# Kernel tuning notes

Measured on AMD Instinct MI355X. Metric: run time of the kernel, lower is better.

Reference implementation:

```python
import jax, jax.numpy as jnp
import numpy as np


def _lstm_scan(x, mask, W_ih, W_hh, h0, c0):
    # x: [B,S,D], mask: [B,S] bool. Masked LSTM (bias=False, PyTorch gate order i,f,g,o).
    def step(carry, inp):
        h, c = carry
        xt, mt = inp
        gates = xt @ W_ih.T + h @ W_hh.T          # [B, 4H]
        i, f, g, o = jnp.split(gates, 4, axis=-1)
        c_new = jax.nn.sigmoid(f) * c + jax.nn.sigmoid(i) * jnp.tanh(g)
        h_new = jax.nn.sigmoid(o) * jnp.tanh(c_new)
        m = mt[:, None]
        h = jnp.where(m, h_new, h)
        c = jnp.where(m, c_new, c)
        return (h, c), h
    (hT, cT), hs = jax.lax.scan(step, (h0, c0), (x.swapaxes(0, 1), mask.T))
    return hs.swapaxes(0, 1), hT, cT  # [B,S,H], [B,H], [B,H]


def setup_inputs() -> dict:
    key = jax.random.key(0)
    ks = jax.random.split(key, 24)
    B, S, V, E, H, DA, R, MH = 64, 1024, 50000, 300, 256, 64, 16, 512
    N_ET, N_PRT, N_POPT = 50, 12, 8
    sc = 1.0 / np.sqrt(H)
    input_ids = jax.random.randint(ks[0], (B, S), 0, V)
    len_li = jnp.sort(jax.random.randint(ks[1], (B,), S // 2, S + 1))[::-1]  # descending, >=1
    inp = {
        'input_ids': input_ids,
        'len_li': len_li,
        'h0': jnp.zeros((2, B, H), jnp.float32),
        'c0': jnp.zeros((2, B, H), jnp.float32),
        'emb': jax.random.normal(ks[2], (V, E), jnp.float32) * 0.1,
        'W_ih_f': jax.random.normal(ks[3], (4 * H, E), jnp.float32) * sc,
        'W_hh_f': jax.random.normal(ks[4], (4 * H, H), jnp.float32) * sc,
        'W_ih_b': jax.random.normal(ks[5], (4 * H, E), jnp.float32) * sc,
        'W_hh_b': jax.random.normal(ks[6], (4 * H, H), jnp.float32) * sc,
        'S1': jax.random.uniform(ks[7], (DA, 2 * H), jnp.float32, -0.1, 0.1),
        'S2': jax.random.uniform(ks[8], (R, DA), jnp.float32, -0.1, 0.1),
        'W_et': jax.random.uniform(ks[9], (MH, R * 2 * H), jnp.float32, -0.1, 0.1),
        'b_et': jnp.zeros((MH,), jnp.float32),
        'Wd_et': jax.random.uniform(ks[10], (N_ET, MH), jnp.float32, -0.1, 0.1),
        'bd_et': jnp.zeros((N_ET,), jnp.float32),
        'W_prt': jax.random.uniform(ks[11], (MH, R * 2 * H), jnp.float32, -0.1, 0.1),
        'b_prt': jnp.zeros((MH,), jnp.float32),
        'Wd_prt': jax.random.uniform(ks[12], (N_PRT, MH), jnp.float32, -0.1, 0.1),
        'bd_prt': jnp.zeros((N_PRT,), jnp.float32),
        'W_popt': jax.random.uniform(ks[13], (MH, R * 2 * H), jnp.float32, -0.1, 0.1),
        'b_popt': jnp.zeros((MH,), jnp.float32),
        'Wd_popt': jax.random.uniform(ks[14], (N_POPT, MH), jnp.float32, -0.1, 0.1),
        'bd_popt': jnp.zeros((N_POPT,), jnp.float32),
    }
    return inp


def reference(input_ids, len_li, h0, c0, emb, W_ih_f, W_hh_f, W_ih_b, W_hh_b,
              S1, S2, W_et, b_et, Wd_et, bd_et, W_prt, b_prt, Wd_prt, bd_prt,
              W_popt, b_popt, Wd_popt, bd_popt):
    B, S = input_ids.shape
    t = jnp.arange(S)[None, :]
    mask = t < len_li[:, None]                                  # [B,S]
    x = emb[input_ids]                                          # [B,S,E]
    # forward direction
    out_f, hf, cf = _lstm_scan(x, mask, W_ih_f, W_hh_f, h0[0], c0[0])
    # backward direction: reverse each sequence within its own length (involution)
    rev_idx = jnp.clip(len_li[:, None] - 1 - t, 0, S - 1)       # [B,S]
    x_rev = jnp.take_along_axis(x, rev_idx[:, :, None], axis=1)
    out_b_rev, hb, cb = _lstm_scan(x_rev, mask, W_ih_b, W_hh_b, h0[1], c0[1])
    out_b = jnp.take_along_axis(out_b_rev, rev_idx[:, :, None], axis=1)
    Hout = jnp.concatenate([out_f, out_b], axis=-1)             # [B,S,2H]
    # self-attention: A = softmax over valid positions, per row of r
    s2 = jnp.tanh(Hout @ S1.T) @ S2.T                           # [B,S,r]
    NEG = jnp.asarray(-1e30, Hout.dtype)
    scores = jnp.where(mask[:, :, None], s2, NEG).swapaxes(1, 2)  # [B,r,S]
    A = jax.nn.softmax(scores, axis=-1)                         # [B,r,S]
    M = jnp.einsum('brs,bsd->brd', A, Hout)                     # [B,r,2H]
    BM = M.reshape(B, -1)                                       # [B, r*2H]
    AAT = jnp.einsum('brs,bqs->brq', A, A)                      # [B,r,r]
    I = jnp.eye(A.shape[1], dtype=A.dtype)
    penal = jnp.mean(jnp.sum((AAT - I) ** 2, axis=(1, 2)))      # mean ||AA^T - I||_F^2
    def head(W, b, Wd, bd):
        return jax.nn.relu(BM @ W.T + b) @ Wd.T + bd
    decoded_et = head(W_et, b_et, Wd_et, bd_et)
    decoded_prt = head(W_prt, b_prt, Wd_prt, bd_prt)
    decoded_popt = head(W_popt, b_popt, Wd_popt, bd_popt)
    hidden = (jnp.stack([hf, hb]), jnp.stack([cf, cb]))
    return (decoded_et, decoded_prt, decoded_popt, hidden, penal, A)
```

## Files before the change

kernel.cpp:

```cpp
#include <hip/hip_runtime.h>
#include <cstdint>
#include <cstddef>

typedef short bf16x8 __attribute__((ext_vector_type(8)));
typedef float f32x4 __attribute__((ext_vector_type(4)));

#define DEVI static __device__ __forceinline__

DEVI unsigned short f2bf(float f) {
  union { float f; unsigned u; } v; v.f = f;
  unsigned r = (v.u + 0x7fffu + ((v.u >> 16) & 1u)) >> 16;
  return (unsigned short)r;
}
DEVI float bf2f(unsigned short s) {
  union { unsigned u; float f; } v; v.u = ((unsigned)s) << 16;
  return v.f;
}
DEVI float sigf(float x) { return 1.f / (1.f + __expf(-x)); }
DEVI float tanh_f(float x) {
  float xc = fminf(fmaxf(x, -15.f), 15.f);
  float e = __expf(2.f * xc);
  return 1.f - 2.f / (e + 1.f);
}
DEVI unsigned long long ldg_sc1_64(const unsigned long long* p) {
  return __hip_atomic_load(p, __ATOMIC_RELAXED, __HIP_MEMORY_SCOPE_AGENT);
}
DEVI void stg_sc1(unsigned* p, unsigned v) {
  __hip_atomic_store(p, v, __ATOMIC_RELAXED, __HIP_MEMORY_SCOPE_AGENT);
}

#define DO_ET     0
#define DO_PRT    3200
#define DO_POPT   3968
#define DO_H      4480
#define DO_C      37248
#define DO_PENAL  70016
#define DO_A      70017

__global__ __launch_bounds__(256) void k_pack(
    const float* __restrict__ Wih_f, const float* __restrict__ Wih_b,
    const float* __restrict__ Whh_f, const float* __restrict__ Whh_b,
    const float* __restrict__ S1,
    unsigned short* __restrict__ BihP, unsigned short* __restrict__ BhhP,
    unsigned short* __restrict__ S1P, int* __restrict__ flags, float* __restrict__ dout)
{
  int idx = blockIdx.x * 256 + threadIdx.x;
  if (idx < 655360) {
    int d = idx / 327680; int e = idx % 327680;
    int j = e & 7; int lane = (e >> 3) & 63;
    int r1 = e >> 9;
    int kc = r1 % 10; int r2 = r1 / 10;
    int mt = r2 & 1; int w = (r2 >> 1) & 3; int ht = r2 >> 3;
    int l15 = lane & 15, quad = lane >> 4;
    int gate = l15 & 3, dimoff = l15 >> 2;
    int dim = ht * 32 + w * 8 + 2 * dimoff + mt;
    int row = gate * 256 + dim;
    int k = kc * 32 + quad * 8 + j;
    const float* W = d ? Wih_b : Wih_f;
    BihP[idx] = f2bf((k < 300) ? W[row * 300 + k] : 0.f);
  } else if (idx < 1179648) {
    int e0 = idx - 655360;
    int d = e0 >> 18; int e = e0 & 262143;
    int j = e & 7; int lane = (e >> 3) & 63;
    int kc = (e >> 9) & 7; int mt = (e >> 12) & 1; int w = (e >> 13) & 3; int ht = (e >> 15) & 7;
    int l15 = lane & 15, quad = lane >> 4;
    int gate = l15 & 3, dimoff = l15 >> 2;
    int dim = ht * 32 + w * 8 + 2 * dimoff + mt;
    int row = gate * 256 + dim;
    int k = kc * 32 + quad * 8 + j;
    const float* W = d ? Whh_b : Whh_f;
    BhhP[e0] = f2bf(W[row * 256 + k]);
  } else if (idx < 1212416) {
    int e = idx - 1179648;
    int j = e & 7; int da = (e >> 3) & 63; int kb = e >> 9;
    S1P[e] = f2bf(S1[da * 512 + kb * 8 + j]);
  } else if (idx < 1213440) {
    flags[idx - 1212416] = 0;
  } else if (idx == 1213440) {
    dout[DO_PENAL] = 0.f;
  }
}

__global__ __launch_bounds__(256, 1) void k_rnn(
    const int* __restrict__ ids, const float* __restrict__ emb,
    const unsigned short* __restrict__ BihP, const unsigned short* __restrict__ BhhP,
    unsigned short* __restrict__ Hbuf, unsigned short* __restrict__ Hout, int* flags,
    const int* __restrict__ len, const float* __restrict__ h0, const float* __restrict__ c0,
    float* __restrict__ dout)
{
  int blk = blockIdx.x;
  int ht = blk >> 3; int g = blk & 7; int d = g >> 2; int bt = g & 3;
  int tid = threadIdx.x;
  int lane = tid & 63, w = tid >> 6, l15 = lane & 15, quad = lane >> 4;
  int b0 = bt * 16;

  __shared__ unsigned short Xl[2][5120];
  __shared__ unsigned short h0p[4096];
  __shared__ int lenS[16];

  const unsigned short* BA = BihP + (size_t)d * 327680;
  const unsigned short* BH = BhhP + (size_t)d * 262144;
  int hw = ht * 4 + w;
  bf16x8 wih[2][10];
  bf16x8 whh[2][8];
  #pragma unroll
  for (int mt = 0; mt < 2; ++mt) {
    #pragma unroll
    for (int kc = 0; kc < 10; ++kc)
      wih[mt][kc] = *reinterpret_cast<const bf16x8*>(
          BA + ((size_t)(((hw * 2 + mt) * 10 + kc) * 64 + lane)) * 8);
    #pragma unroll
    for (int kc = 0; kc < 8; ++kc)
      whh[mt][kc] = *reinterpret_cast<const bf16x8*>(
          BH + ((size_t)(((hw * 2 + mt) * 8 + kc) * 64 + lane)) * 8);
  }

  for (int i = tid; i < 4096; i += 256) {
    int kb = i >> 7, mm = (i >> 3) & 15, j = i & 7;
    h0p[i] = f2bf(h0[d * 16384 + (b0 + mm) * 256 + kb * 8 + j]);
  }
  if (tid < 16) lenS[tid] = len[b0 + tid];
  for (int i = tid; i < 128; i += 256) {
    ((unsigned*)Xl[0])[2432 + i] = 0;
    ((unsigned*)Xl[1])[2432 + i] = 0;
  }
  __syncthreads();

  int xm = tid >> 4, xf = tid & 15;
  {
    int lbm = lenS[xm];
    int s = d ? (lbm - 1) : 0;
    s = s < 0 ? 0 : (s > 1023 ? 1023 : s);
    int tok = ids[(b0 + xm) * 1024 + s];
    const float* er = emb + (size_t)tok * 300;
    #pragma unroll
    for (int i = 0; i < 5; ++i) {
      int f = xf + 16 * i;
      float4 v = (f <= 74) ? *reinterpret_cast<const float4*>(er + 4 * f)
                           : (float4){0.f, 0.f, 0.f, 0.f};
      if (f < 76) {
        int uo = ((f >> 1) * 16 + xm) * 4 + (f & 1) * 2;
        ((unsigned*)Xl[0])[uo]     = (unsigned)f2bf(v.x) | ((unsigned)f2bf(v.y) << 16);
        ((unsigned*)Xl[0])[uo + 1] = (unsigned)f2bf(v.z) | ((unsigned)f2bf(v.w) << 16);
      }
    }
  }
  __syncthreads();

  int len_my = lenS[l15];
  int Tmax = lenS[0];
  int k0 = ht * 32 + w * 8 + 2 * quad;
  int cidx = d * 16384 + (b0 + l15) * 256 + k0;
  float cc0 = c0[cidx], cc1 = c0[cidx + 1];
  float hh0 = h0[cidx], hh1 = h0[cidx + 1];

  unsigned short* HbufG = Hbuf + (size_t)g * 8192;
  int* fl = flags + g * 128;

  for (int t = 0; t < Tmax; ++t) {
    float4 xr[5];
    {
      int tn = t + 1;
      int s = d ? (lenS[xm] - 1 - tn) : tn;
      s = s < 0 ? 0 : (s > 1023 ? 1023 : s);
      int tok = ids[(b0 + xm) * 1024 + s];
      const float* er = emb + (size_t)tok * 300;
      #pragma unroll
      for (int i = 0; i < 5; ++i) {
        int f = xf + 16 * i;
        xr[i] = (f <= 74) ? *reinterpret_cast<const float4*>(er + 4 * f)
                          : (float4){0.f, 0.f, 0.f, 0.f};
      }
    }

    f32x4 a0 = {0.f, 0.f, 0.f, 0.f}, a1 = {0.f, 0.f, 0.f, 0.f};
    {
      const unsigned short* Xb = Xl[t & 1];
      #pragma unroll
      for (int kc = 0; kc < 10; ++kc) {
        bf16x8 bx = *reinterpret_cast<const bf16x8*>(&Xb[((kc * 4 + quad) * 16 + l15) * 8]);
        a0 = __builtin_amdgcn_mfma_f32_16x16x32_bf16(wih[0][kc], bx, a0, 0, 0, 0);
        a1 = __builtin_amdgcn_mfma_f32_16x16x32_bf16(wih[1][kc], bx, a1, 0, 0, 0);
      }
    }

    bf16x8 ah[8];
    if (t == 0) {
      #pragma unroll
      for (int kc = 0; kc < 8; ++kc)
        ah[kc] = *reinterpret_cast<const bf16x8*>(&h0p[((kc * 4 + quad) * 16 + l15) * 8]);
    } else {
      int polls = 0;
      while (true) {
        int v = 0x7fffffff;
        if (lane < 8)
          v = __hip_atomic_load(fl + lane * 16, __ATOMIC_RELAXED, __HIP_MEMORY_SCOPE_AGENT);
        if (__ballot(v >= t) == ~0ull) break;
        if (++polls > 100000) break;
      }
      asm volatile("" ::: "memory");
      const unsigned long long* slotU =
          (const unsigned long long*)(HbufG + (size_t)(t & 1) * 4096);
      #pragma unroll
      for (int kc = 0; kc < 8; ++kc) {
        int qo = (((kc * 4 + quad) * 16 + l15) * 4) >> 1;
        union { unsigned long long q[2]; bf16x8 v; } tu;
        tu.q[0] = ldg_sc1_64(slotU + qo);
        tu.q[1] = ldg_sc1_64(slotU + qo + 1);
        ah[kc] = tu.v;
      }
    }
    #pragma unroll
    for (int kc = 0; kc < 8; ++kc) {
      a0 = __builtin_amdgcn_mfma_f32_16x16x32_bf16(whh[0][kc], ah[kc], a0, 0, 0, 0);
      a1 = __builtin_amdgcn_mfma_f32_16x16x32_bf16(whh[1][kc], ah[kc], a1, 0, 0, 0);
    }

    if (t < len_my) {
      float cn0 = sigf(a0[1]) * cc0 + sigf(a0[0]) * tanh_f(a0[2]);
      cc0 = cn0; hh0 = sigf(a0[3]) * tanh_f(cn0);
      float cn1 = sigf(a1[1]) * cc1 + sigf(a1[0]) * tanh_f(a1[2]);
      cc1 = cn1; hh1 = sigf(a1[3]) * tanh_f(cn1);
    }

    unsigned hp = (unsigned)f2bf(hh0) | ((unsigned)f2bf(hh1) << 16);
    stg_sc1((unsigned*)(HbufG + (size_t)((t + 1) & 1) * 4096) + (hw * 64 + l15 * 4 + quad), hp);

    {
      unsigned* LX = (unsigned*)Xl[(t + 1) & 1];
      #pragma unroll
      for (int i = 0; i < 5; ++i) {
        int f = xf + 16 * i;
        if (f < 76) {
          int uo = ((f >> 1) * 16 + xm) * 4 + (f & 1) * 2;
          LX[uo]     = (unsigned)f2bf(xr[i].x) | ((unsigned)f2bf(xr[i].y) << 16);
          LX[uo + 1] = (unsigned)f2bf(xr[i].z) | ((unsigned)f2bf(xr[i].w) << 16);
        }
      }
    }

    __syncthreads();
    if (tid == 0)
      __hip_atomic_store(fl + ht * 16, t + 1, __ATOMIC_RELAXED, __HIP_MEMORY_SCOPE_AGENT);

    size_t hob = (size_t)(b0 + l15) * 524288;
    if (d == 0) {
      *reinterpret_cast<unsigned*>(Hout + hob + (size_t)t * 512 + k0) = hp;
    } else if (t < len_my) {
      *reinterpret_cast<unsigned*>(Hout + hob + (size_t)(len_my - 1 - t) * 512 + 256 + k0) = hp;
    }
    if (t == len_my - 1) {
      dout[DO_H + cidx] = hh0; dout[DO_H + cidx + 1] = hh1;
      dout[DO_C + cidx] = cc0; dout[DO_C + cidx + 1] = cc1;
    }
  }
}

__global__ __launch_bounds__(256, 2) void k_scores(
    const unsigned short* __restrict__ Hout, const unsigned short* __restrict__ S1P,
    const float* __restrict__ S2, float* __restrict__ scores)
{
  __shared__ float U[128 * 65];
  __shared__ float S2l[16 * 65];
  int tid = threadIdx.x;
  int t0 = blockIdx.x * 128;
  int b = blockIdx.y;
  int lane = tid & 63, w = tid >> 6, l15 = lane & 15, quad = lane >> 4;

  f32x4 acc[2][4];
  #pragma unroll
  for (int i = 0; i < 2; ++i)
    #pragma unroll
    for (int j = 0; j < 4; ++j) acc[i][j] = (f32x4){0.f, 0.f, 0.f, 0.f};

  for (int kc = 0; kc < 16; ++kc) {
    bf16x8 afr[2];
    #pragma unroll
    for (int mt = 0; mt < 2; ++mt) {
      int row = t0 + w * 32 + mt * 16 + l15;
      afr[mt] = *reinterpret_cast<const bf16x8*>(
          Hout + (size_t)b * 524288 + (size_t)row * 512 + kc * 32 + quad * 8);
    }
    bf16x8 bfr[4];
    #pragma unroll
    for (int nt = 0; nt < 4; ++nt)
      bfr[nt] = *reinterpret_cast<const bf16x8*>(
          S1P + ((size_t)(kc * 4 + quad) * 64 + nt * 16 + l15) * 8);
    #pragma unroll
    for (int mt = 0; mt < 2; ++mt)
      #pragma unroll
      for (int nt = 0; nt < 4; ++nt)
        acc[mt][nt] = __builtin_amdgcn_mfma_f32_16x16x32_bf16(afr[mt], bfr[nt], acc[mt][nt], 0, 0, 0);
  }
  #pragma unroll
  for (int mt = 0; mt < 2; ++mt)
    #pragma unroll
    for (int nt = 0; nt < 4; ++nt)
      #pragma unroll
      for (int r = 0; r < 4; ++r)
        U[(w * 32 + mt * 16 + quad * 4 + r) * 65 + nt * 16 + l15] = acc[mt][nt][r];
  for (int i = tid; i < 1024; i += 256) S2l[(i >> 6) * 65 + (i & 63)] = S2[i];
  __syncthreads();
  for (int i = tid; i < 8192; i += 256) {
    int row = i >> 6, c = i & 63;
    U[row * 65 + c] = tanh_f(U[row * 65 + c]);
  }
  __syncthreads();
  for (int idx = tid; idx < 2048; idx += 256) {
    int row = idx >> 4, r = idx & 15;
    float s = 0.f;
    #pragma unroll 8
    for (int da = 0; da < 64; ++da) s += U[row * 65 + da] * S2l[r * 65 + da];
    scores[((size_t)b * 16 + r) * 1024 + t0 + row] = s;
  }
}

__global__ __launch_bounds__(256) void k_softmax(
    const float* __restrict__ scores, const int* __restrict__ len, float* __restrict__ dout)
{
  __shared__ float red[256];
  int b = blockIdx.x, r = blockIdx.y;
  int tid = threadIdx.x;
  int lb = len[b];
  const float* src = scores + ((size_t)b * 16 + r) * 1024;
  float v[4]; float mx = -3.0e38f;
  #pragma unroll
  for (int i = 0; i < 4; ++i) {
    int t = tid + i * 256;
    v[i] = (t < lb) ? src[t] : -3.0e38f;
    mx = fmaxf(mx, v[i]);
  }
  red[tid] = mx; __syncthreads();
  for (int s = 128; s > 0; s >>= 1) { if (tid < s) red[tid] = fmaxf(red[tid], red[tid + s]); __syncthreads(); }
  float M = red[0]; __syncthreads();
  float se = 0.f;
  #pragma unroll
  for (int i = 0; i < 4; ++i) {
    int t = tid + i * 256;
    if (t < lb) { v[i] = __expf(v[i] - M); se += v[i]; }
  }
  red[tid] = se; __syncthreads();
  for (int s = 128; s > 0; s >>= 1) { if (tid < s) red[tid] += red[tid + s]; __syncthreads(); }
  float inv = 1.f / red[0];
  float* dst = dout + DO_A + ((size_t)b * 16 + r) * 1024;
  #pragma unroll
  for (int i = 0; i < 4; ++i) {
    int t = tid + i * 256;
    dst[t] = (t < lb) ? v[i] * inv : 0.f;
  }
}

__global__ __launch_bounds__(256) void k_penal(float* __restrict__ dout)
{
  __shared__ float Al[16 * 513];
  __shared__ float red[256];
  int b = blockIdx.x, tid = threadIdx.x;
  const float* A = dout + DO_A + (size_t)b * 16384;
  int r = tid >> 4, q = tid & 15;
  float s = 0.f;
  for (int half = 0; half < 2; ++half) {
    __syncthreads();
    for (int i = tid; i < 8192; i += 256) {
      int rr = i >> 9, t = i & 511;
      Al[rr * 513 + t] = A[rr * 1024 + half * 512 + t];
    }
    __syncthreads();
    for (int t = 0; t < 512; ++t) s += Al[r * 513 + t] * Al[q * 513 + t];
  }
  float dv = s - ((r == q) ? 1.f : 0.f);
  red[tid] = dv * dv; __syncthreads();
  for (int st = 128; st > 0; st >>= 1) { if (tid < st) red[tid] += red[tid + st]; __syncthreads(); }
  if (tid == 0) atomicAdd(dout + DO_PENAL, red[0] * (1.f / 64.f));
}

__global__ __launch_bounds__(256) void k_attnM(
    const float* __restrict__ dout, const unsigned short* __restrict__ Hout,
    const int* __restrict__ len, float* __restrict__ Mws)
{
  int b = blockIdx.x, dc = blockIdx.y;
  int tid = threadIdx.x;
  int col = dc * 128 + (tid & 127);
  int rh = tid >> 7;
  int lb = len[b];
  const float* Ab = dout + DO_A + (size_t)b * 16384;
  const unsigned short* Hb = Hout + (size_t)b * 524288;
  float acc[8];
  #pragma unroll
  for (int i = 0; i < 8; ++i) acc[i] = 0.f;
  for (int t = 0; t < lb; ++t) {
    float h = bf2f(Hb[(size_t)t * 512 + col]);
    #pragma unroll
    for (int rr = 0; rr < 8; ++rr) acc[rr] += Ab[(rh * 8 + rr) * 1024 + t] * h;
  }
  #pragma unroll
  for (int rr = 0; rr < 8; ++rr) Mws[(size_t)b * 8192 + (rh * 8 + rr) * 512 + col] = acc[rr];
}

__global__ __launch_bounds__(256) void k_heads1(
    const float* __restrict__ W, const float* __restrict__ Mws, float* __restrict__ P)
{
  int tid = threadIdx.x;
  int n = blockIdx.x * 16 + (tid & 15);
  int ks = blockIdx.y;
  int bg = tid >> 4;
  const float* Wr = W + (size_t)n * 8192 + ks * 1024;
  float acc[4] = {0.f, 0.f, 0.f, 0.f};
  for (int k = 0; k < 1024; k += 4) {
    float4 wv = *reinterpret_cast<const float4*>(Wr + k);
    #pragma unroll
    for (int i = 0; i < 4; ++i) {
      float4 mv = *reinterpret_cast<const float4*>(Mws + (size_t)(bg * 4 + i) * 8192 + ks * 1024 + k);
      acc[i] += wv.x * mv.x + wv.y * mv.y + wv.z * mv.z + wv.w * mv.w;
    }
  }
  #pragma unroll
  for (int i = 0; i < 4; ++i)
    P[(size_t)(ks * 64 + bg * 4 + i) * 512 + n] = acc[i];
}

__global__ __launch_bounds__(256) void k_headred(
    const float* __restrict__ Pws, const float* __restrict__ b_et,
    const float* __restrict__ b_prt, const float* __restrict__ b_popt,
    float* __restrict__ hid)
{
  int idx = blockIdx.x * 256 + threadIdx.x;
  int head = idx >> 15; int rem = idx & 32767;
  int b = rem >> 9; int n = rem & 511;
  const float* bias = (head == 0) ? b_et : (head == 1) ? b_prt : b_popt;
  float s = bias[n];
  #pragma unroll
  for (int ks = 0; ks < 8; ++ks)
    s += Pws[(size_t)(head * 8 + ks) * 32768 + b * 512 + n];
  hid[idx] = fmaxf(s, 0.f);
}

__global__ __launch_bounds__(256) void k_head2(
    const float* __restrict__ hid, const float* __restrict__ Wd, const float* __restrict__ bd,
    float* __restrict__ out, int No)
{
  int idx = blockIdx.x * 256 + threadIdx.x;
  if (idx >= 64 * No) return;
  int b = idx / No, o = idx % No;
  const float* hv = hid + (size_t)b * 512;
  const float* wr = Wd + (size_t)o * 512;
  float acc = bd[o];
  for (int k = 0; k < 512; k += 4) {
    float4 h4 = *reinterpret_cast<const float4*>(hv + k);
    float4 w4 = *reinterpret_cast<const float4*>(wr + k);
    acc += h4.x * w4.x + h4.y * w4.y + h4.z * w4.z + h4.w * w4.w;
  }
  out[idx] = acc;
}

extern "C" void kernel_launch(void* const* d_in, const int* in_sizes, int n_in,
                              void* d_out, int out_size, void* d_ws, size_t ws_size,
                              hipStream_t stream) {
  const int*   ids    = (const int*)d_in[0];
  const int*   len    = (const int*)d_in[1];
  const float* h0     = (const float*)d_in[2];
  const float* c0     = (const float*)d_in[3];
  const float* emb    = (const float*)d_in[4];
  const float* Wih_f  = (const float*)d_in[5];
  const float* Whh_f  = (const float*)d_in[6];
  const float* Wih_b  = (const float*)d_in[7];
  const float* Whh_b  = (const float*)d_in[8];
  const float* S1     = (const float*)d_in[9];
  const float* S2     = (const float*)d_in[10];
  const float* W_et   = (const float*)d_in[11];
  const float* b_et   = (const float*)d_in[12];
  const float* Wd_et  = (const float*)d_in[13];
  const float* bd_et  = (const float*)d_in[14];
  const float* W_prt  = (const float*)d_in[15];
  const float* b_prt  = (const float*)d_in[16];
  const float* Wd_prt = (const float*)d_in[17];
  const float* bd_prt = (const float*)d_in[18];
  const float* W_popt = (const float*)d_in[19];
  const float* b_popt = (const float*)d_in[20];
  const float* Wd_popt= (const float*)d_in[21];
  const float* bd_popt= (const float*)d_in[22];
  float* dout = (float*)d_out;
  char* ws = (char*)d_ws;

  size_t off = 0;
  auto AL = [&](size_t bytes) { size_t r = off; off += (bytes + 255) & ~(size_t)255; return r; };
  size_t oHout = AL(67108864UL);
  size_t oBih  = AL(1310720UL);
  size_t oBhh  = AL(1048576UL);
  size_t oS1P  = AL(65536UL);
  size_t oHbuf = AL(131072UL);
  size_t oFlag = AL(4096UL);
  size_t oPws  = AL(3145728UL);
  size_t oSc   = AL(4194304UL);
  size_t oM    = oSc;
  size_t oHid  = oSc + 2097152UL;

  unsigned short* Hout = (unsigned short*)(ws + oHout);
  unsigned short* BihP = (unsigned short*)(ws + oBih);
  unsigned short* BhhP = (unsigned short*)(ws + oBhh);
  unsigned short* S1P  = (unsigned short*)(ws + oS1P);
  unsigned short* Hbuf = (unsigned short*)(ws + oHbuf);
  int* flags           = (int*)(ws + oFlag);
  float* Pws           = (float*)(ws + oPws);
  float* scores        = (float*)(ws + oSc);
  float* Mws           = (float*)(ws + oM);
  float* hid           = (float*)(ws + oHid);

  hipLaunchKernelGGL(k_pack, dim3(4741), dim3(256), 0, stream,
                     Wih_f, Wih_b, Whh_f, Whh_b, S1, BihP, BhhP, S1P, flags, dout);
  hipLaunchKernelGGL(k_rnn, dim3(64), dim3(256), 0, stream,
                     ids, emb, BihP, BhhP, Hbuf, Hout, flags, len, h0, c0, dout);
  hipLaunchKernelGGL(k_scores, dim3(8, 64), dim3(256), 0, stream, Hout, S1P, S2, scores);
  hipLaunchKernelGGL(k_softmax, dim3(64, 16), dim3(256), 0, stream, scores, len, dout);
  hipLaunchKernelGGL(k_penal, dim3(64), dim3(256), 0, stream, dout);
  hipLaunchKernelGGL(k_attnM, dim3(64, 4), dim3(256), 0, stream, dout, Hout, len, Mws);
  hipLaunchKernelGGL(k_heads1, dim3(32, 8), dim3(256), 0, stream, W_et,   Mws, Pws);
  hipLaunchKernelGGL(k_heads1, dim3(32, 8), dim3(256), 0, stream, W_prt,  Mws, Pws + 262144);
  hipLaunchKernelGGL(k_heads1, dim3(32, 8), dim3(256), 0, stream, W_popt, Mws, Pws + 524288);
  hipLaunchKernelGGL(k_headred, dim3(384), dim3(256), 0, stream, Pws, b_et, b_prt, b_popt, hid);
  hipLaunchKernelGGL(k_head2, dim3(13), dim3(256), 0, stream, hid,         Wd_et,   bd_et,   dout + DO_ET, 50);
  hipLaunchKernelGGL(k_head2, dim3(3),  dim3(256), 0, stream, hid + 32768, Wd_prt,  bd_prt,  dout + DO_PRT, 12);
  hipLaunchKernelGGL(k_head2, dim3(2),  dim3(256), 0, stream, hid + 65536, Wd_popt, bd_popt, dout + DO_POPT, 8);
}
```

Before: 3.287 ms.

## Load embedding rows directly into MFMA registers with two-step prefetch, drop LDS staging

Each lane now gathers its own embedding slice straight into registers in the MFMA B-operand layout, prefetching two steps ahead and converting to bf16 at the end of each step. This removes the shared-memory X double buffer, the LDS stores and reads, and the initial h0 staging. The cost is redundant global loads, since each of the four waves fetches the same rows, and more register pressure (20 float4 plus 10 bf16x8 per lane) in a kernel that is already heavy on registers. It also still keeps one __syncthreads per step.

```diff
diff --git a/kernel.cpp b/kernel.cpp
--- a/kernel.cpp
+++ b/kernel.cpp
@@ -94,10 +94,6 @@
   int lane = tid & 63, w = tid >> 6, l15 = lane & 15, quad = lane >> 4;
   int b0 = bt * 16;
 
-  __shared__ unsigned short Xl[2][5120];
-  __shared__ unsigned short h0p[4096];
-  __shared__ int lenS[16];
-
   const unsigned short* BA = BihP + (size_t)d * 327680;
   const unsigned short* BH = BhhP + (size_t)d * 262144;
   int hw = ht * 4 + w;
@@ -115,80 +111,71 @@
           BH + ((size_t)(((hw * 2 + mt) * 8 + kc) * 64 + lane)) * 8);
   }
 
-  for (int i = tid; i < 4096; i += 256) {
-    int kb = i >> 7, mm = (i >> 3) & 15, j = i & 7;
-    h0p[i] = f2bf(h0[d * 16384 + (b0 + mm) * 256 + kb * 8 + j]);
-  }
-  if (tid < 16) lenS[tid] = len[b0 + tid];
-  for (int i = tid; i < 128; i += 256) {
-    ((unsigned*)Xl[0])[2432 + i] = 0;
-    ((unsigned*)Xl[1])[2432 + i] = 0;
-  }
-  __syncthreads();
-
-  int xm = tid >> 4, xf = tid & 15;
-  {
-    int lbm = lenS[xm];
-    int s = d ? (lbm - 1) : 0;
-    s = s < 0 ? 0 : (s > 1023 ? 1023 : s);
-    int tok = ids[(b0 + xm) * 1024 + s];
-    const float* er = emb + (size_t)tok * 300;
-    #pragma unroll
-    for (int i = 0; i < 5; ++i) {
-      int f = xf + 16 * i;
-      float4 v = (f <= 74) ? *reinterpret_cast<const float4*>(er + 4 * f)
-                           : (float4){0.f, 0.f, 0.f, 0.f};
-      if (f < 76) {
-        int uo = ((f >> 1) * 16 + xm) * 4 + (f & 1) * 2;
-        ((unsigned*)Xl[0])[uo]     = (unsigned)f2bf(v.x) | ((unsigned)f2bf(v.y) << 16);
-        ((unsigned*)Xl[0])[uo + 1] = (unsigned)f2bf(v.z) | ((unsigned)f2bf(v.w) << 16);
-      }
-    }
-  }
-  __syncthreads();
-
-  int len_my = lenS[l15];
-  int Tmax = lenS[0];
+  int len_my = len[b0 + l15];
+  int Tmax   = len[b0];
   int k0 = ht * 32 + w * 8 + 2 * quad;
   int cidx = d * 16384 + (b0 + l15) * 256 + k0;
   float cc0 = c0[cidx], cc1 = c0[cidx + 1];
   float hh0 = h0[cidx], hh1 = h0[cidx + 1];
 
+  const int* idrow = ids + (size_t)(b0 + l15) * 1024;
+  const float4 FZ = {0.f, 0.f, 0.f, 0.f};
+
+  float4 xr[10][2];
+  bf16x8 bx[10];
+
+  auto issueX = [&](int ts) {
+    int s = d ? (len_my - 1 - ts) : ts;
+    s = s < 0 ? 0 : (s > 1023 ? 1023 : s);
+    int tok = idrow[s];
+    const float* er = emb + (size_t)tok * 300;
+    #pragma unroll
+    for (int kc = 0; kc < 10; ++kc) {
+      int kb = kc * 4 + quad;
+      xr[kc][0] = (kb <= 37) ? *reinterpret_cast<const float4*>(er + kb * 8)     : FZ;
+      xr[kc][1] = (kb <= 36) ? *reinterpret_cast<const float4*>(er + kb * 8 + 4) : FZ;
+    }
+  };
+  auto convX = [&]() {
+    #pragma unroll
+    for (int kc = 0; kc < 10; ++kc) {
+      union { bf16x8 v; unsigned short s[8]; } u;
+      u.s[0] = f2bf(xr[kc][0].x); u.s[1] = f2bf(xr[kc][0].y);
+      u.s[2] = f2bf(xr[kc][0].z); u.s[3] = f2bf(xr[kc][0].w);
+      u.s[4] = f2bf(xr[kc][1].x); u.s[5] = f2bf(xr[kc][1].y);
+      u.s[6] = f2bf(xr[kc][1].z); u.s[7] = f2bf(xr[kc][1].w);
+      bx[kc] = u.v;
+    }
+  };
+
+  issueX(0);
+  convX();
+  issueX(1);
+
   unsigned short* HbufG = Hbuf + (size_t)g * 8192;
   int* fl = flags + g * 128;
 
   for (int t = 0; t < Tmax; ++t) {
-    float4 xr[5];
-    {
-      int tn = t + 1;
-      int s = d ? (lenS[xm] - 1 - tn) : tn;
-      s = s < 0 ? 0 : (s > 1023 ? 1023 : s);
-      int tok = ids[(b0 + xm) * 1024 + s];
-      const float* er = emb + (size_t)tok * 300;
-      #pragma unroll
-      for (int i = 0; i < 5; ++i) {
-        int f = xf + 16 * i;
-        xr[i] = (f <= 74) ? *reinterpret_cast<const float4*>(er + 4 * f)
-                          : (float4){0.f, 0.f, 0.f, 0.f};
-      }
-    }
-
     f32x4 a0 = {0.f, 0.f, 0.f, 0.f}, a1 = {0.f, 0.f, 0.f, 0.f};
-    {
-      const unsigned short* Xb = Xl[t & 1];
-      #pragma unroll
-      for (int kc = 0; kc < 10; ++kc) {
-        bf16x8 bx = *reinterpret_cast<const bf16x8*>(&Xb[((kc * 4 + quad) * 16 + l15) * 8]);
-        a0 = __builtin_amdgcn_mfma_f32_16x16x32_bf16(wih[0][kc], bx, a0, 0, 0, 0);
-        a1 = __builtin_amdgcn_mfma_f32_16x16x32_bf16(wih[1][kc], bx, a1, 0, 0, 0);
-      }
+    #pragma unroll
+    for (int kc = 0; kc < 10; ++kc) {
+      a0 = __builtin_amdgcn_mfma_f32_16x16x32_bf16(wih[0][kc], bx[kc], a0, 0, 0, 0);
+      a1 = __builtin_amdgcn_mfma_f32_16x16x32_bf16(wih[1][kc], bx[kc], a1, 0, 0, 0);
     }
 
     bf16x8 ah[8];
     if (t == 0) {
+      const float* hb = h0 + d * 16384 + (size_t)(b0 + l15) * 256;
       #pragma unroll
-      for (int kc = 0; kc < 8; ++kc)
-        ah[kc] = *reinterpret_cast<const bf16x8*>(&h0p[((kc * 4 + quad) * 16 + l15) * 8]);
+      for (int kc = 0; kc < 8; ++kc) {
+        int kb = kc * 4 + quad;
+        float4 a = *reinterpret_cast<const float4*>(hb + kb * 8);
+        float4 b = *reinterpret_cast<const float4*>(hb + kb * 8 + 4);
+        union { bf16x8 v; unsigned short s[8]; } u;
+        u.s[0] = f2bf(a.x); u.s[1] = f2bf(a.y); u.s[2] = f2bf(a.z); u.s[3] = f2bf(a.w);
+        u.s[4] = f2bf(b.x); u.s[5] = f2bf(b.y); u.s[6] = f2bf(b.z); u.s[7] = f2bf(b.w);
+        ah[kc] = u.v;
+      }
     } else {
       int polls = 0;
       while (true) {
@@ -226,19 +213,6 @@
     unsigned hp = (unsigned)f2bf(hh0) | ((unsigned)f2bf(hh1) << 16);
     stg_sc1((unsigned*)(HbufG + (size_t)((t + 1) & 1) * 4096) + (hw * 64 + l15 * 4 + quad), hp);
 
-    {
-      unsigned* LX = (unsigned*)Xl[(t + 1) & 1];
-      #pragma unroll
-      for (int i = 0; i < 5; ++i) {
-        int f = xf + 16 * i;
-        if (f < 76) {
-          int uo = ((f >> 1) * 16 + xm) * 4 + (f & 1) * 2;
-          LX[uo]     = (unsigned)f2bf(xr[i].x) | ((unsigned)f2bf(xr[i].y) << 16);
-          LX[uo + 1] = (unsigned)f2bf(xr[i].z) | ((unsigned)f2bf(xr[i].w) << 16);
-        }
-      }
-    }
-
     __syncthreads();
     if (tid == 0)
       __hip_atomic_store(fl + ht * 16, t + 1, __ATOMIC_RELAXED, __HIP_MEMORY_SCOPE_AGENT);
@@ -253,6 +227,9 @@
       dout[DO_H + cidx] = hh0; dout[DO_H + cidx + 1] = hh1;
       dout[DO_C + cidx] = cc0; dout[DO_C + cidx + 1] = cc1;
     }
+
+    convX();
+    issueX(t + 2);
   }
 }
 
```

Result: slower. 4.521 ms (+37.5%).
